# Kernel tuning notes

Measured on AMD Instinct MI355X. Metric: run time of the kernel, lower is better.

## Reference

```python
import jax, jax.numpy as jnp
import numpy as np

N, E, C, A, R = 8192, 65536, 64, 16, 8
DIMS = (1, 3, 5, 7)        # dims of l = 0..3 irrep blocks
IRDIM = sum(DIMS)          # 16
L = len(DIMS)              # 4 TP paths (0e x l -> l, 'uvu')
WN = L * C                 # conv_tp weight_numel = 256
HID = 64                   # radial MLP hidden width
AVG_NUM_NEIGH = 16.0


def setup_inputs() -> dict:
    key = jax.random.key(0)
    ks = jax.random.split(key, 18)
    f = lambda k, s: jax.random.normal(k, s, dtype=jnp.float32)
    return dict(
        node_attrs=f(ks[0], (N, A)),
        node_feats=f(ks[1], (N, C)),
        edge_attrs=f(ks[2], (E, IRDIM)),
        edge_feats=f(ks[3], (E, R)),
        edge_index=jax.random.randint(ks[4], (2, E), 0, N),
        magmom_node_inv_feats=f(ks[5], (N, R)),
        magmom_node_attrs=f(ks[6], (N, IRDIM)),
        # learned parameters (e3nn-style, no biases, 1/sqrt(fan_in) path norm)
        W_up=f(ks[7], (C, C)),
        W_r0=f(ks[8], (R + R, HID)),
        W_r1=f(ks[9], (HID, HID)),
        W_r2=f(ks[10], (HID, HID)),
        W_r3=f(ks[11], (HID, WN)),
        W_trans=f(ks[12], (WN, WN)),
        W_dens=f(ks[13], (R, 1)),
        W_lin=f(ks[14], (L, C, C)),
        W_mlin=f(ks[15], (L, C, C)),
        W_skip=f(ks[16], (L, C, A, C)),
        W_mskip=f(ks[17], (L, C, A, C)),
    )


def _per_l_linear(x, W):
    # equivariant Linear: independent channel-mixing per l block. x: [N,C,16]
    outs, o = [], 0
    for l, d in enumerate(DIMS):
        outs.append(jnp.einsum('ncm,cd->ndm', x[:, :, o:o + d], W[l]) / np.sqrt(C))
        o += d
    return jnp.concatenate(outs, axis=-1)


def _skip_tp(x, attrs, W):
    # FullyConnectedTensorProduct with scalar (0e) node attrs: (l x 0e -> l, 'uvw')
    outs, o = [], 0
    for l, d in enumerate(DIMS):
        outs.append(jnp.einsum('num,nv,uvw->nwm', x[:, :, o:o + d], attrs, W[l]) / np.sqrt(C * A))
        o += d
    return jnp.concatenate(outs, axis=-1)


def _weighted_tp(xj, attrs_e, w):
    # weighted TP of 0e node feats with lmax=3 attrs: per-edge 'uvu' weights.
    # xj: [E,C], attrs_e: [E,16], w: [E,L,C] -> [E,C,16]
    wf = jnp.repeat(w, np.array(DIMS), axis=1, total_repeat_length=IRDIM)  # [E,16,C]
    return xj[:, :, None] * attrs_e[:, None, :] * jnp.swapaxes(wf, 1, 2)


def reference(node_attrs, node_feats, edge_attrs, edge_feats, edge_index,
              magmom_node_inv_feats, magmom_node_attrs,
              W_up, W_r0, W_r1, W_r2, W_r3, W_trans, W_dens,
              W_lin, W_mlin, W_skip, W_mskip):
    sender, receiver = edge_index[0], edge_index[1]
    x = node_feats @ W_up / np.sqrt(C)                     # linear_up (0e)
    xj = x[sender]                                         # gather by sender
    h = jnp.concatenate([edge_feats, magmom_node_inv_feats[sender]], axis=-1)
    for W in (W_r0, W_r1, W_r2):                           # radial MLP (silu)
        h = jax.nn.silu(h @ W / np.sqrt(W.shape[0]))
    tp_w = (h @ W_r3 / np.sqrt(HID)).reshape(E, L, C)      # per-edge TP weights
    edge_density = jnp.tanh((edge_feats @ W_dens / np.sqrt(R)) ** 2)  # [E,1]
    mji = _weighted_tp(xj, edge_attrs, tp_w)               # [E,C,16]
    tp_w_m = (tp_w.reshape(E, WN) @ W_trans / np.sqrt(WN)).reshape(E, L, C)
    magmom_mji = _weighted_tp(xj, magmom_node_attrs[sender], tp_w_m)
    density = jax.ops.segment_sum(edge_density, receiver, num_segments=N)       # [N,1]
    message = jax.ops.segment_sum(mji, receiver, num_segments=N)                # [N,C,16]
    magmom_message = jax.ops.segment_sum(magmom_mji, receiver, num_segments=N)
    message = _per_l_linear(message, W_lin) / (density[:, :, None] + 1.0)
    message = _skip_tp(message, node_attrs, W_skip)
    magmom_message = _per_l_linear(magmom_message, W_mlin) / AVG_NUM_NEIGH
    magmom_message = _skip_tp(magmom_message, node_attrs, W_mskip)
    return message, magmom_message                         # each [N,C,16] (reshape_irreps layout)
```

## Files before the change

kernel.cpp:

```cpp
#include <hip/hip_runtime.h>

#define N_NODES 8192
#define N_EDGES 65536

typedef __attribute__((ext_vector_type(8))) short bf16x8;
typedef __attribute__((ext_vector_type(4))) float f32x4;

static __device__ __forceinline__ float bfl(unsigned v){ unsigned u=v<<16; float f; __builtin_memcpy(&f,&u,4); return f; }
static __device__ __forceinline__ float bfh(unsigned v){ unsigned u=v&0xffff0000u; float f; __builtin_memcpy(&f,&u,4); return f; }
static __device__ __forceinline__ float bfs(unsigned short h){ unsigned u=((unsigned)h)<<16; float f; __builtin_memcpy(&f,&u,4); return f; }
static __device__ __forceinline__ unsigned short f2bf(float f){ unsigned u; __builtin_memcpy(&u,&f,4); u += 0x7fffu + ((u>>16)&1u); return (unsigned short)(u>>16); }
static __device__ __forceinline__ unsigned pk(float a, float b){ return (unsigned)f2bf(a) | ((unsigned)f2bf(b)<<16); }
static __device__ __forceinline__ float silu_f(float v){ return v/(1.f+__expf(-v)); }

__global__ __launch_bounds__(256) void k_linup(const float* __restrict__ nf,
                                               const float* __restrict__ wup,
                                               float* __restrict__ x){
    __shared__ float s[4][64];
    const int t=threadIdx.x, wv=t>>6, lane=t&63;
    const int n=blockIdx.x*4+wv;
    s[wv][lane]=nf[(size_t)n*64+lane];
    __syncthreads();
    float acc=0.f;
    for(int c=0;c<64;++c) acc += s[wv][c]*wup[c*64+lane];
    x[(size_t)n*64+lane]=acc*0.125f;
}

__global__ __launch_bounds__(256) void k_wmlp(const float* __restrict__ wr0,
                                              const float* __restrict__ wr1,
                                              const float* __restrict__ wr2,
                                              unsigned short* __restrict__ w0f,
                                              unsigned short* __restrict__ w1f,
                                              unsigned short* __restrict__ w2f){
    const int b=blockIdx.x, t=threadIdx.x;
    #pragma unroll
    for(int z=0;z<2;++z){
        int idx=t*2+z;
        int lane=idx>>3, i=idx&7;
        if(b<4){
            int nt=b, k=(lane>>4)*8+i, n=nt*16+(lane&15);
            float v=(k<16)? wr0[k*64+n]*0.25f : 0.f;
            w0f[(nt*64+lane)*8+i]=f2bf(v);
        } else if(b<12){
            int q=b-4, nt=q>>1, ks=q&1;
            int k=ks*32+(lane>>4)*8+i, n=nt*16+(lane&15);
            w1f[((nt*2+ks)*64+lane)*8+i]=f2bf(wr1[k*64+n]*0.125f);
        } else {
            int q=b-12, nt=q>>1, ks=q&1;
            int k=ks*32+(lane>>4)*8+i, n=nt*16+(lane&15);
            w2f[((nt*2+ks)*64+lane)*8+i]=f2bf(wr2[k*64+n]*0.125f);
        }
    }
}

__global__ __launch_bounds__(256) void k_wtf(const float* __restrict__ wr3,
                                             const float* __restrict__ wtr,
                                             unsigned short* __restrict__ wtf){
    const int b=blockIdx.x;
    const int mt=b>>1, ks=b&1, t=threadIdx.x;
    #pragma unroll
    for(int z=0;z<2;++z){
        int idx=t*2+z;
        int lane=idx>>3, i=idx&7;
        int k=ks*32+(lane>>4)*8+i;
        int n=mt*16+(lane&15);
        int j=n>>3, s=n&7;
        float v;
        if(s<4) v=wr3[k*256+s*64+j]*0.125f;
        else {
            float acc=0.f;
            for(int kk=0;kk<256;++kk) acc+=wr3[k*256+kk]*wtr[kk*256+(s-4)*64+j];
            v=acc*(1.f/128.f);
        }
        wtf[((size_t)b*64+lane)*8+i]=f2bf(v);
    }
}

__global__ __launch_bounds__(256) void k_wwf(const float* __restrict__ wlin,
                                             const float* __restrict__ wmlin,
                                             const float* __restrict__ wskip,
                                             const float* __restrict__ wmskip,
                                             unsigned* __restrict__ wwf){
    const int b=blockIdx.x, ten=b>>8, lc=b&255, l=lc>>6, c=lc&63;
    const float* WL = ten? wmlin:wlin;
    const float* WS = ten? wmskip:wskip;
    const float scale = ten? (1.f/4096.f):(1.f/256.f);
    const int t=threadIdx.x, wg=t>>6, s=t&63, lane=s>>1, half=s&1;
    const int kg=lane>>4, w=wg*16+(lane&15);
    const int v0=kg*8+half*4;
    float a0=0,a1=0,a2=0,a3=0;
    for(int u=0;u<64;++u){
        float wl=WL[(l*64+c)*64+u];
        const float* wsp=&WS[(((l*64+u)*16+v0)*64)+w];
        a0+=wl*wsp[0]; a1+=wl*wsp[64]; a2+=wl*wsp[128]; a3+=wl*wsp[192];
    }
    size_t fi=(((size_t)ten*4+l)*64+c)*4+wg;
    unsigned* op=wwf + (fi*32+lane)*4 + half*2;
    op[0]=pk(a0*scale,a1*scale); op[1]=pk(a2*scale,a3*scale);
}

__global__ __launch_bounds__(256) void k_count(const int* __restrict__ recv, int* __restrict__ cnt){
    int e=blockIdx.x*256+threadIdx.x;
    atomicAdd(&cnt[recv[e]],1);
}
__global__ __launch_bounds__(1024) void k_scan(const int* __restrict__ cnt, int* __restrict__ rowptr, int* __restrict__ cur){
    __shared__ int s[1024];
    const int t=threadIdx.x;
    int c[8]; int sum=0;
    #pragma unroll
    for(int i=0;i<8;++i){ c[i]=cnt[t*8+i]; sum+=c[i]; }
    s[t]=sum; __syncthreads();
    for(int off=1;off<1024;off<<=1){
        int v=s[t]; int add=(t>=off)? s[t-off]:0;
        __syncthreads();
        s[t]=v+add;
        __syncthreads();
    }
    int run=s[t]-sum;
    #pragma unroll
    for(int i=0;i<8;++i){ rowptr[t*8+i]=run; cur[t*8+i]=run; run+=c[i]; }
    if(t==1023) rowptr[8192]=run;
}
__global__ __launch_bounds__(256) void k_scatter(const int* __restrict__ recv, int* __restrict__ cur, int* __restrict__ elist){
    int e=blockIdx.x*256+threadIdx.x;
    int r=recv[e];
    int p=atomicAdd(&cur[r],1);
    elist[p]=e;
}

__global__ __launch_bounds__(256) void k_edge2(
    const float* __restrict__ ef, const float* __restrict__ mminv,
    const float* __restrict__ mattr, const int* __restrict__ sender,
    const float* __restrict__ wdens,
    const uint4* __restrict__ w0f, const uint4* __restrict__ w1f,
    const uint4* __restrict__ w2f, const uint4* __restrict__ wtf,
    const float* __restrict__ x,
    unsigned short* __restrict__ wxc, float* __restrict__ man, float* __restrict__ ed)
{
    __shared__ unsigned short hA[4096];
    __shared__ unsigned short hB[4096];
    __shared__ float xs[64*68];
    const int t=threadIdx.x, lane=t&63, wv=t>>6;
    const int tile=blockIdx.x*64;

    {
        const int e=t>>2, q=t&3, ge=tile+e;
        const int s=sender[ge];
        const float4* xp=(const float4*)(x+(size_t)s*64+q*16);
        float4* xw=(float4*)&xs[e*68+q*16];
        xw[0]=xp[0]; xw[1]=xp[1]; xw[2]=xp[2]; xw[3]=xp[3];
        *(float4*)(man+(size_t)ge*16+q*4) = *(const float4*)(mattr+(size_t)s*16+q*4);
        const int se3=(e&7)<<3;
        if(q==0){
            float4 f0=*(const float4*)(ef+(size_t)ge*8);
            float4 f1=*(const float4*)(ef+(size_t)ge*8+4);
            uint4 o; o.x=pk(f0.x,f0.y); o.y=pk(f0.z,f0.w); o.z=pk(f1.x,f1.y); o.w=pk(f1.z,f1.w);
            *(uint4*)&hA[e*64 + (0^se3)]=o;
            float acc=f0.x*wdens[0]+f0.y*wdens[1]+f0.z*wdens[2]+f0.w*wdens[3]
                     +f1.x*wdens[4]+f1.y*wdens[5]+f1.z*wdens[6]+f1.w*wdens[7];
            acc*=0.35355339059327373f;
            float q2=acc*acc;
            float ex=__expf(2.f*q2);
            ed[ge]=1.f-2.f/(ex+1.f);
        } else if(q==1){
            float4 f0=*(const float4*)(mminv+(size_t)s*8);
            float4 f1=*(const float4*)(mminv+(size_t)s*8+4);
            uint4 o; o.x=pk(f0.x,f0.y); o.y=pk(f0.z,f0.w); o.z=pk(f1.x,f1.y); o.w=pk(f1.z,f1.w);
            *(uint4*)&hA[e*64 + (8^se3)]=o;
        } else if(q==2){
            *(uint4*)&hA[e*64 + (16^se3)]=make_uint4(0,0,0,0);
        } else {
            *(uint4*)&hA[e*64 + (24^se3)]=make_uint4(0,0,0,0);
        }
    }
    __syncthreads();

    const int arow=wv*16+(lane&15);
    const int akg=lane>>4;
    const int aswz=(arow&7)<<3;
    const int dcol=lane&15;
    const int drow0=wv*16+(lane>>4)*4;

    {
        uint4 av=*(const uint4*)&hA[arow*64+((akg*8)^aswz)];
        bf16x8 a; __builtin_memcpy(&a,&av,16);
        f32x4 d[4];
        #pragma unroll
        for(int nt=0;nt<4;++nt){
            uint4 bw=w0f[nt*64+lane];
            bf16x8 b; __builtin_memcpy(&b,&bw,16);
            f32x4 z={0.f,0.f,0.f,0.f};
            d[nt]=__builtin_amdgcn_mfma_f32_16x16x32_bf16(a,b,z,0,0,0);
        }
        #pragma unroll
        for(int nt=0;nt<4;++nt){
            #pragma unroll
            for(int r=0;r<4;++r){
                int e2=drow0+r, n=nt*16+dcol;
                hB[e2*64 + (n^((e2&7)<<3))]=f2bf(silu_f(d[nt][r]));
            }
        }
    }
    __syncthreads();

    {
        uint4 av0=*(const uint4*)&hB[arow*64+(((0+akg)*8)^aswz)];
        uint4 av1=*(const uint4*)&hB[arow*64+(((4+akg)*8)^aswz)];
        bf16x8 a0,a1; __builtin_memcpy(&a0,&av0,16); __builtin_memcpy(&a1,&av1,16);
        f32x4 d[4];
        #pragma unroll
        for(int nt=0;nt<4;++nt){
            uint4 bw0=w1f[(nt*2+0)*64+lane];
            uint4 bw1=w1f[(nt*2+1)*64+lane];
            bf16x8 b0,b1; __builtin_memcpy(&b0,&bw0,16); __builtin_memcpy(&b1,&bw1,16);
            f32x4 z={0.f,0.f,0.f,0.f};
            d[nt]=__builtin_amdgcn_mfma_f32_16x16x32_bf16(a0,b0,z,0,0,0);
            d[nt]=__builtin_amdgcn_mfma_f32_16x16x32_bf16(a1,b1,d[nt],0,0,0);
        }
        #pragma unroll
        for(int nt=0;nt<4;++nt){
            #pragma unroll
            for(int r=0;r<4;++r){
                int e2=drow0+r, n=nt*16+dcol;
                hA[e2*64 + (n^((e2&7)<<3))]=f2bf(silu_f(d[nt][r]));
            }
        }
    }
    __syncthreads();

    {
        uint4 av0=*(const uint4*)&hA[arow*64+(((0+akg)*8)^aswz)];
        uint4 av1=*(const uint4*)&hA[arow*64+(((4+akg)*8)^aswz)];
        bf16x8 a0,a1; __builtin_memcpy(&a0,&av0,16); __builtin_memcpy(&a1,&av1,16);
        f32x4 d[4];
        #pragma unroll
        for(int nt=0;nt<4;++nt){
            uint4 bw0=w2f[(nt*2+0)*64+lane];
            uint4 bw1=w2f[(nt*2+1)*64+lane];
            bf16x8 b0,b1; __builtin_memcpy(&b0,&bw0,16); __builtin_memcpy(&b1,&bw1,16);
            f32x4 z={0.f,0.f,0.f,0.f};
            d[nt]=__builtin_amdgcn_mfma_f32_16x16x32_bf16(a0,b0,z,0,0,0);
            d[nt]=__builtin_amdgcn_mfma_f32_16x16x32_bf16(a1,b1,d[nt],0,0,0);
        }
        #pragma unroll
        for(int nt=0;nt<4;++nt){
            #pragma unroll
            for(int r=0;r<4;++r){
                int e2=drow0+r, n=nt*16+dcol;
                hB[e2*64 + (n^((e2&7)<<3))]=f2bf(silu_f(d[nt][r]));
            }
        }
    }
    __syncthreads();

    {
        bf16x8 hb[4][2];
        #pragma unroll
        for(int nt2=0;nt2<4;++nt2){
            int erow=nt2*16+(lane&15);
            int esz=(erow&7)<<3;
            #pragma unroll
            for(int ks=0;ks<2;++ks){
                uint4 v=*(const uint4*)&hB[erow*64+(((ks*4+akg)*8)^esz)];
                __builtin_memcpy(&hb[nt2][ks],&v,16);
            }
        }
        const int g=lane>>4;
        const int jo=g>>1, sh=g&1;
        for(int mt=0;mt<8;++mt){
            int mtg=wv*8+mt;
            uint4 aw0=wtf[(mtg*2+0)*64+lane];
            uint4 aw1=wtf[(mtg*2+1)*64+lane];
            bf16x8 a0,a1; __builtin_memcpy(&a0,&aw0,16); __builtin_memcpy(&a1,&aw1,16);
            int j=mtg*2+jo;
            #pragma unroll
            for(int nt2=0;nt2<4;++nt2){
                f32x4 z={0.f,0.f,0.f,0.f};
                f32x4 d=__builtin_amdgcn_mfma_f32_16x16x32_bf16(a0,hb[nt2][0],z,0,0,0);
                d=__builtin_amdgcn_mfma_f32_16x16x32_bf16(a1,hb[nt2][1],d,0,0,0);
                int eloc=nt2*16+(lane&15);
                float xj=xs[eloc*68+j];
                uint2 o; o.x=pk(d[0]*xj,d[1]*xj); o.y=pk(d[2]*xj,d[3]*xj);
                *(uint2*)&wxc[((size_t)(tile+eloc)*64+j)*8+sh*4]=o;
            }
        }
    }
}

__global__ __launch_bounds__(256) void k_gather(
    const int* __restrict__ rowptr, const int* __restrict__ elist,
    const unsigned short* __restrict__ wxc, const float* __restrict__ ea,
    const float* __restrict__ man, const float* __restrict__ ed,
    float* __restrict__ out)
{
    const int t=threadIdx.x, wv=t>>6, lane=t&63;
    const int n=blockIdx.x*4+wv;
    const int r0=rowptr[n], r1=rowptr[n+1];
    float msg[16]; float mm[16];
    #pragma unroll
    for(int m=0;m<16;++m){ msg[m]=0.f; mm[m]=0.f; }
    float dens=0.f;
    for(int k=r0;k<r1;++k){
        int e=elist[k];
        uint4 r=*(const uint4*)(wxc+((size_t)e*64+lane)*8);
        float wx0=bfl(r.x),wx1=bfh(r.x),wx2=bfl(r.y),wx3=bfh(r.y);
        float wm0=bfl(r.z),wm1=bfh(r.z),wm2=bfl(r.w),wm3=bfh(r.w);
        dens+=ed[e];
        const float4* eap=(const float4*)(ea+(size_t)e*16);
        const float4* map=(const float4*)(man+(size_t)e*16);
        float4 A0=eap[0],A1=eap[1],A2=eap[2],A3=eap[3];
        float4 B0=map[0],B1=map[1],B2=map[2],B3=map[3];
        msg[0]+=wx0*A0.x;
        msg[1]+=wx1*A0.y;  msg[2]+=wx1*A0.z;  msg[3]+=wx1*A0.w;
        msg[4]+=wx2*A1.x;  msg[5]+=wx2*A1.y;  msg[6]+=wx2*A1.z;  msg[7]+=wx2*A1.w;  msg[8]+=wx2*A2.x;
        msg[9]+=wx3*A2.y;  msg[10]+=wx3*A2.z; msg[11]+=wx3*A2.w;
        msg[12]+=wx3*A3.x; msg[13]+=wx3*A3.y; msg[14]+=wx3*A3.z; msg[15]+=wx3*A3.w;
        mm[0]+=wm0*B0.x;
        mm[1]+=wm1*B0.y;  mm[2]+=wm1*B0.z;  mm[3]+=wm1*B0.w;
        mm[4]+=wm2*B1.x;  mm[5]+=wm2*B1.y;  mm[6]+=wm2*B1.z;  mm[7]+=wm2*B1.w;  mm[8]+=wm2*B2.x;
        mm[9]+=wm3*B2.y;  mm[10]+=wm3*B2.z; mm[11]+=wm3*B2.w;
        mm[12]+=wm3*B3.x; mm[13]+=wm3*B3.y; mm[14]+=wm3*B3.z; mm[15]+=wm3*B3.w;
    }
    float inv=1.f/(1.f+dens);
    float* mp=out+(size_t)n*1024+lane*16;
    ((float4*)mp)[0]=make_float4(msg[0]*inv,msg[1]*inv,msg[2]*inv,msg[3]*inv);
    ((float4*)mp)[1]=make_float4(msg[4]*inv,msg[5]*inv,msg[6]*inv,msg[7]*inv);
    ((float4*)mp)[2]=make_float4(msg[8]*inv,msg[9]*inv,msg[10]*inv,msg[11]*inv);
    ((float4*)mp)[3]=make_float4(msg[12]*inv,msg[13]*inv,msg[14]*inv,msg[15]*inv);
    float* qp=out+8388608+(size_t)n*1024+lane*16;
    ((float4*)qp)[0]=make_float4(mm[0],mm[1],mm[2],mm[3]);
    ((float4*)qp)[1]=make_float4(mm[4],mm[5],mm[6],mm[7]);
    ((float4*)qp)[2]=make_float4(mm[8],mm[9],mm[10],mm[11]);
    ((float4*)qp)[3]=make_float4(mm[12],mm[13],mm[14],mm[15]);
}

__global__ __launch_bounds__(256) void k_final6(const float* __restrict__ attrs,
                                                const unsigned* __restrict__ wwf,
                                                float* __restrict__ out){
    __shared__ unsigned short msgS[64*16*8];
    const int blk=blockIdx.x;
    const int half=blk&1;
    const int rest=blk>>1;
    const int ten=rest>>9, nb=(rest&511)*16;
    float* base=out+(size_t)ten*8388608;
    const int t=threadIdx.x, lane=t&63, wg=t>>6;
    const int L0=half;

    const float4* src=(const float4*)(base+(size_t)nb*1024);
    #pragma unroll
    for(int i=0;i<8;++i){
        int tau=i*256+t;
        int n=tau>>7, rem=tau&127, c=rem>>1, qq=rem&1;
        float4 f=src[(n<<8)+(c<<2)+half*2+qq];
        unsigned* dst=(unsigned*)&msgS[(c*16+n)*8+qq*4];
        dst[0]=pk(f.x,f.y); dst[1]=pk(f.z,f.w);
    }
    bf16x8 afrag;
    {
        int nloc=lane&15, kg=lane>>4;
        if(kg<2){
            const float* ap=attrs+(size_t)(nb+nloc)*16+kg*8;
            #pragma unroll
            for(int i=0;i<8;++i) afrag[i]=(short)f2bf(ap[i]);
        } else {
            #pragma unroll
            for(int i=0;i<8;++i) afrag[i]=0;
        }
    }
    __syncthreads();

    const int g4=(lane>>4)*4;
    const int colw=lane&15;
    float acc[4][8];
    #pragma unroll
    for(int r=0;r<4;++r)
        #pragma unroll
        for(int m=0;m<8;++m) acc[r][m]=0.f;

    const uint4* wwf4=(const uint4*)wwf;
    uint4 bcur[3], bnxt[3];
    #pragma unroll
    for(int li=0;li<3;++li){
        int fi=(((ten*4+L0+li)*64+0)*4+wg);
        bcur[li]=wwf4[fi*32+(lane&31)];
    }

    constexpr int LI0[8]={0,1,1,1,2,2,2,2};
    constexpr int LI1[8]={1,2,2,2,2,2,2,2};

    for(int c=0;c<64;++c){
        if(c<63){
            #pragma unroll
            for(int li=0;li<3;++li){
                int fi=(((ten*4+L0+li)*64+(c+1))*4+wg);
                bnxt[li]=wwf4[fi*32+(lane&31)];
            }
        }
        f32x4 d[3];
        #pragma unroll
        for(int li=0;li<3;++li){
            bf16x8 b; __builtin_memcpy(&b,&bcur[li],16);
            f32x4 z={0.f,0.f,0.f,0.f};
            d[li]=__builtin_amdgcn_mfma_f32_16x16x32_bf16(afrag,b,z,0,0,0);
        }
        #pragma unroll
        for(int r=0;r<4;++r){
            uint4 h=*(const uint4*)&msgS[(c*16+g4+r)*8];
            unsigned wd[4]={h.x,h.y,h.z,h.w};
            #pragma unroll
            for(int m=0;m<8;++m){
                float mv = (m&1)? bfh(wd[m>>1]) : bfl(wd[m>>1]);
                float dv = half? d[LI1[m]][r] : d[LI0[m]][r];
                acc[r][m] += mv * dv;
            }
        }
        if(c<63){
            #pragma unroll
            for(int li=0;li<3;++li) bcur[li]=bnxt[li];
        }
    }
    const int w=wg*16+colw;
    #pragma unroll
    for(int r=0;r<4;++r){
        float* op=base+(size_t)(nb+g4+r)*1024+w*16+half*8;
        ((float4*)op)[0]=make_float4(acc[r][0],acc[r][1],acc[r][2],acc[r][3]);
        ((float4*)op)[1]=make_float4(acc[r][4],acc[r][5],acc[r][6],acc[r][7]);
    }
}

extern "C" void kernel_launch(void* const* d_in, const int* in_sizes, int n_in,
                              void* d_out, int out_size, void* d_ws, size_t ws_size,
                              hipStream_t stream) {
    const float* node_attrs=(const float*)d_in[0];
    const float* node_feats=(const float*)d_in[1];
    const float* edge_attrs=(const float*)d_in[2];
    const float* edge_feats=(const float*)d_in[3];
    const int*   eidx_in  =(const int*)  d_in[4];
    const int*   sender   =eidx_in;
    const int*   recv     =eidx_in+N_EDGES;
    const float* mminv    =(const float*)d_in[5];
    const float* mattr    =(const float*)d_in[6];
    const float* wup      =(const float*)d_in[7];
    const float* wr0      =(const float*)d_in[8];
    const float* wr1      =(const float*)d_in[9];
    const float* wr2      =(const float*)d_in[10];
    const float* wr3      =(const float*)d_in[11];
    const float* wtr      =(const float*)d_in[12];
    const float* wdens    =(const float*)d_in[13];
    const float* wlin     =(const float*)d_in[14];
    const float* wmlin    =(const float*)d_in[15];
    const float* wskip    =(const float*)d_in[16];
    const float* wmskip   =(const float*)d_in[17];

    char* ws=(char*)d_ws;
    float*          x     =(float*)(ws+0);
    unsigned short* wxc   =(unsigned short*)(ws+2097152);
    float*          man   =(float*)(ws+69206016);
    float*          ed    =(float*)(ws+73400320);
    unsigned short* wtf   =(unsigned short*)(ws+73662464);
    unsigned*       wwf   =(unsigned*)(ws+73728000);
    unsigned short* w0f   =(unsigned short*)(ws+75825152);
    unsigned short* w1f   =(unsigned short*)(ws+75829248);
    unsigned short* w2f   =(unsigned short*)(ws+75837440);
    int*            cnt   =(int*)(ws+75845632);
    int*            rowptr=(int*)(ws+75878400);
    int*            cur   =(int*)(ws+75911296);
    int*            elist =(int*)(ws+75944064);
    if(ws_size < (size_t)76206208) return;

    float* out=(float*)d_out;

    hipMemsetAsync(cnt,0,32768,stream);
    k_linup  <<<dim3(2048),dim3(256),0,stream>>>(node_feats,wup,x);
    k_wmlp   <<<dim3(20),  dim3(256),0,stream>>>(wr0,wr1,wr2,w0f,w1f,w2f);
    k_wtf    <<<dim3(64),  dim3(256),0,stream>>>(wr3,wtr,wtf);
    k_wwf    <<<dim3(512), dim3(256),0,stream>>>(wlin,wmlin,wskip,wmskip,wwf);
    k_count  <<<dim3(256), dim3(256),0,stream>>>(recv,cnt);
    k_scan   <<<dim3(1),   dim3(1024),0,stream>>>(cnt,rowptr,cur);
    k_scatter<<<dim3(256), dim3(256),0,stream>>>(recv,cur,elist);
    k_edge2  <<<dim3(1024),dim3(256),0,stream>>>(edge_feats,mminv,mattr,sender,wdens,
                                                 (const uint4*)w0f,(const uint4*)w1f,
                                                 (const uint4*)w2f,(const uint4*)wtf,
                                                 x,wxc,man,ed);
    k_gather <<<dim3(2048),dim3(256),0,stream>>>(rowptr,elist,wxc,edge_attrs,man,ed,out);
    k_final6 <<<dim3(2048),dim3(256),0,stream>>>(node_attrs,wwf,out);
}
```

Measured before the change: 259.2 us.

## Drop per-edge magmom attr copy, precompute W_r3·W_trans, restructure final skip kernel

Measured after the change: 242.1 us. 1.07x faster.

```diff
diff --git a/kernel.cpp b/kernel.cpp
--- a/kernel.cpp
+++ b/kernel.cpp
@@ -53,8 +53,17 @@
     }
 }
 
+__global__ __launch_bounds__(256) void k_w3t(const float* __restrict__ wr3,
+                                             const float* __restrict__ wtr,
+                                             float* __restrict__ wt){
+    const int k=blockIdx.x, n=threadIdx.x;
+    float acc=0.f;
+    for(int kk=0;kk<256;++kk) acc += wr3[k*256+kk]*wtr[kk*256+n];
+    wt[k*256+n]=acc;
+}
+
 __global__ __launch_bounds__(256) void k_wtf(const float* __restrict__ wr3,
-                                             const float* __restrict__ wtr,
+                                             const float* __restrict__ wt,
                                              unsigned short* __restrict__ wtf){
     const int b=blockIdx.x;
     const int mt=b>>1, ks=b&1, t=threadIdx.x;
@@ -65,13 +74,8 @@
         int k=ks*32+(lane>>4)*8+i;
         int n=mt*16+(lane&15);
         int j=n>>3, s=n&7;
-        float v;
-        if(s<4) v=wr3[k*256+s*64+j]*0.125f;
-        else {
-            float acc=0.f;
-            for(int kk=0;kk<256;++kk) acc+=wr3[k*256+kk]*wtr[kk*256+(s-4)*64+j];
-            v=acc*(1.f/128.f);
-        }
+        float v = (s<4)? wr3[k*256+s*64+j]*0.125f
+                       : wt[k*256+(s-4)*64+j]*(1.f/128.f);
         wtf[((size_t)b*64+lane)*8+i]=f2bf(v);
     }
 }
@@ -130,12 +134,12 @@
 
 __global__ __launch_bounds__(256) void k_edge2(
     const float* __restrict__ ef, const float* __restrict__ mminv,
-    const float* __restrict__ mattr, const int* __restrict__ sender,
+    const int* __restrict__ sender,
     const float* __restrict__ wdens,
     const uint4* __restrict__ w0f, const uint4* __restrict__ w1f,
     const uint4* __restrict__ w2f, const uint4* __restrict__ wtf,
     const float* __restrict__ x,
-    unsigned short* __restrict__ wxc, float* __restrict__ man, float* __restrict__ ed)
+    unsigned short* __restrict__ wxc, float* __restrict__ ed)
 {
     __shared__ unsigned short hA[4096];
     __shared__ unsigned short hB[4096];
@@ -149,7 +153,6 @@
         const float4* xp=(const float4*)(x+(size_t)s*64+q*16);
         float4* xw=(float4*)&xs[e*68+q*16];
         xw[0]=xp[0]; xw[1]=xp[1]; xw[2]=xp[2]; xw[3]=xp[3];
-        *(float4*)(man+(size_t)ge*16+q*4) = *(const float4*)(mattr+(size_t)s*16+q*4);
         const int se3=(e&7)<<3;
         if(q==0){
             float4 f0=*(const float4*)(ef+(size_t)ge*8);
@@ -290,7 +293,8 @@
 __global__ __launch_bounds__(256) void k_gather(
     const int* __restrict__ rowptr, const int* __restrict__ elist,
     const unsigned short* __restrict__ wxc, const float* __restrict__ ea,
-    const float* __restrict__ man, const float* __restrict__ ed,
+    const float* __restrict__ mattr, const int* __restrict__ sender,
+    const float* __restrict__ ed,
     float* __restrict__ out)
 {
     const int t=threadIdx.x, wv=t>>6, lane=t&63;
@@ -303,11 +307,12 @@
     for(int k=r0;k<r1;++k){
         int e=elist[k];
         uint4 r=*(const uint4*)(wxc+((size_t)e*64+lane)*8);
+        int s=sender[e];
         float wx0=bfl(r.x),wx1=bfh(r.x),wx2=bfl(r.y),wx3=bfh(r.y);
         float wm0=bfl(r.z),wm1=bfh(r.z),wm2=bfl(r.w),wm3=bfh(r.w);
         dens+=ed[e];
         const float4* eap=(const float4*)(ea+(size_t)e*16);
-        const float4* map=(const float4*)(man+(size_t)e*16);
+        const float4* map=(const float4*)(mattr+(size_t)s*16);
         float4 A0=eap[0],A1=eap[1],A2=eap[2],A3=eap[3];
         float4 B0=map[0],B1=map[1],B2=map[2],B3=map[3];
         msg[0]+=wx0*A0.x;
@@ -334,7 +339,40 @@
     ((float4*)qp)[3]=make_float4(mm[12],mm[13],mm[14],mm[15]);
 }
 
-__global__ __launch_bounds__(256) void k_final6(const float* __restrict__ attrs,
+#define STEP0_(v0,v1,v2, cc) { \
+    _Pragma("unroll") \
+    for(int r_=0;r_<4;++r_){ \
+        uint4 h_=*(const uint4*)&msgS[(((cc)*16+g4+r_))*8]; \
+        float dr0_=v0[r_], dr1_=v1[r_], dr2_=v2[r_]; \
+        acc[r_][0]+=bfl(h_.x)*dr0_; \
+        acc[r_][1]+=bfh(h_.x)*dr1_; \
+        acc[r_][2]+=bfl(h_.y)*dr1_; \
+        acc[r_][3]+=bfh(h_.y)*dr1_; \
+        acc[r_][4]+=bfl(h_.z)*dr2_; \
+        acc[r_][5]+=bfh(h_.z)*dr2_; \
+        acc[r_][6]+=bfl(h_.w)*dr2_; \
+        acc[r_][7]+=bfh(h_.w)*dr2_; \
+    } }
+#define STEP1_(v0,v1, cc) { \
+    _Pragma("unroll") \
+    for(int r_=0;r_<4;++r_){ \
+        uint4 h_=*(const uint4*)&msgS[(((cc)*16+g4+r_))*8]; \
+        float dr0_=v0[r_], dr1_=v1[r_]; \
+        acc[r_][0]+=bfl(h_.x)*dr0_; \
+        acc[r_][1]+=bfh(h_.x)*dr1_; \
+        acc[r_][2]+=bfl(h_.y)*dr1_; \
+        acc[r_][3]+=bfh(h_.y)*dr1_; \
+        acc[r_][4]+=bfl(h_.z)*dr1_; \
+        acc[r_][5]+=bfh(h_.z)*dr1_; \
+        acc[r_][6]+=bfl(h_.w)*dr1_; \
+        acc[r_][7]+=bfh(h_.w)*dr1_; \
+    } }
+#define MFMA1_(o, b) { \
+    bf16x8 f_; __builtin_memcpy(&f_,&(b),16); \
+    f32x4 z_={0.f,0.f,0.f,0.f}; \
+    o=__builtin_amdgcn_mfma_f32_16x16x32_bf16(afrag,f_,z_,0,0,0); }
+
+__global__ __launch_bounds__(256) void k_final8(const float* __restrict__ attrs,
                                                 const unsigned* __restrict__ wwf,
                                                 float* __restrict__ out){
     __shared__ unsigned short msgS[64*16*8];
@@ -344,7 +382,6 @@
     const int ten=rest>>9, nb=(rest&511)*16;
     float* base=out+(size_t)ten*8388608;
     const int t=threadIdx.x, lane=t&63, wg=t>>6;
-    const int L0=half;
 
     const float4* src=(const float4*)(base+(size_t)nb*1024);
     #pragma unroll
@@ -370,7 +407,6 @@
     __syncthreads();
 
     const int g4=(lane>>4)*4;
-    const int colw=lane&15;
     float acc[4][8];
     #pragma unroll
     for(int r=0;r<4;++r)
@@ -378,48 +414,46 @@
         for(int m=0;m<8;++m) acc[r][m]=0.f;
 
     const uint4* wwf4=(const uint4*)wwf;
-    uint4 bcur[3], bnxt[3];
-    #pragma unroll
-    for(int li=0;li<3;++li){
-        int fi=(((ten*4+L0+li)*64+0)*4+wg);
-        bcur[li]=wwf4[fi*32+(lane&31)];
-    }
-
-    constexpr int LI0[8]={0,1,1,1,2,2,2,2};
-    constexpr int LI1[8]={1,2,2,2,2,2,2,2};
-
-    for(int c=0;c<64;++c){
-        if(c<63){
-            #pragma unroll
-            for(int li=0;li<3;++li){
-                int fi=(((ten*4+L0+li)*64+(c+1))*4+wg);
-                bnxt[li]=wwf4[fi*32+(lane&31)];
-            }
-        }
-        f32x4 d[3];
-        #pragma unroll
-        for(int li=0;li<3;++li){
-            bf16x8 b; __builtin_memcpy(&b,&bcur[li],16);
-            f32x4 z={0.f,0.f,0.f,0.f};
-            d[li]=__builtin_amdgcn_mfma_f32_16x16x32_bf16(afrag,b,z,0,0,0);
-        }
-        #pragma unroll
-        for(int r=0;r<4;++r){
-            uint4 h=*(const uint4*)&msgS[(c*16+g4+r)*8];
-            unsigned wd[4]={h.x,h.y,h.z,h.w};
-            #pragma unroll
-            for(int m=0;m<8;++m){
-                float mv = (m&1)? bfh(wd[m>>1]) : bfl(wd[m>>1]);
-                float dv = half? d[LI1[m]][r] : d[LI0[m]][r];
-                acc[r][m] += mv * dv;
-            }
-        }
-        if(c<63){
-            #pragma unroll
-            for(int li=0;li<3;++li) bcur[li]=bnxt[li];
-        }
-    }
-    const int w=wg*16+colw;
+    const int l31=lane&31;
+
+    if(half==0){
+        const uint4* p0=wwf4+((size_t)((ten*4+0)*64)*4+wg)*32+l31;
+        const uint4* p1=wwf4+((size_t)((ten*4+1)*64)*4+wg)*32+l31;
+        const uint4* p2=wwf4+((size_t)((ten*4+2)*64)*4+wg)*32+l31;
+        uint4 A0=p0[0], A1=p1[0], A2=p2[0];
+        uint4 B0=p0[128], B1=p1[128], B2=p2[128];
+        f32x4 dA0,dA1,dA2, dB0,dB1,dB2;
+        MFMA1_(dA0,A0); MFMA1_(dA1,A1); MFMA1_(dA2,A2);
+        for(int c=0;c<64;c+=2){
+            const int cA=(c+2<64)? c+2 : 63;
+            const int cB=(c+3<64)? c+3 : 63;
+            A0=p0[cA*128]; A1=p1[cA*128]; A2=p2[cA*128];
+            MFMA1_(dB0,B0); MFMA1_(dB1,B1); MFMA1_(dB2,B2);
+            STEP0_(dA0,dA1,dA2, c);
+            B0=p0[cB*128]; B1=p1[cB*128]; B2=p2[cB*128];
+            MFMA1_(dA0,A0); MFMA1_(dA1,A1); MFMA1_(dA2,A2);
+            STEP0_(dB0,dB1,dB2, c+1);
+        }
+    } else {
+        const uint4* p0=wwf4+((size_t)((ten*4+2)*64)*4+wg)*32+l31;
+        const uint4* p1=wwf4+((size_t)((ten*4+3)*64)*4+wg)*32+l31;
+        uint4 A0=p0[0], A1=p1[0];
+        uint4 B0=p0[128], B1=p1[128];
+        f32x4 dA0,dA1, dB0,dB1;
+        MFMA1_(dA0,A0); MFMA1_(dA1,A1);
+        for(int c=0;c<64;c+=2){
+            const int cA=(c+2<64)? c+2 : 63;
+            const int cB=(c+3<64)? c+3 : 63;
+            A0=p0[cA*128]; A1=p1[cA*128];
+            MFMA1_(dB0,B0); MFMA1_(dB1,B1);
+            STEP1_(dA0,dA1, c);
+            B0=p0[cB*128]; B1=p1[cB*128];
+            MFMA1_(dA0,A0); MFMA1_(dA1,A1);
+            STEP1_(dB0,dB1, c+1);
+        }
+    }
+
+    const int w=wg*16+(lane&15);
     #pragma unroll
     for(int r=0;r<4;++r){
         float* op=base+(size_t)(nb+g4+r)*1024+w*16+half*8;
@@ -455,7 +489,7 @@
     char* ws=(char*)d_ws;
     float*          x     =(float*)(ws+0);
     unsigned short* wxc   =(unsigned short*)(ws+2097152);
-    float*          man   =(float*)(ws+69206016);
+    float*          wt    =(float*)(ws+69206016);
     float*          ed    =(float*)(ws+73400320);
     unsigned short* wtf   =(unsigned short*)(ws+73662464);
     unsigned*       wwf   =(unsigned*)(ws+73728000);
@@ -473,15 +507,16 @@
     hipMemsetAsync(cnt,0,32768,stream);
     k_linup  <<<dim3(2048),dim3(256),0,stream>>>(node_feats,wup,x);
     k_wmlp   <<<dim3(20),  dim3(256),0,stream>>>(wr0,wr1,wr2,w0f,w1f,w2f);
-    k_wtf    <<<dim3(64),  dim3(256),0,stream>>>(wr3,wtr,wtf);
+    k_w3t    <<<dim3(64),  dim3(256),0,stream>>>(wr3,wtr,wt);
+    k_wtf    <<<dim3(64),  dim3(256),0,stream>>>(wr3,wt,wtf);
     k_wwf    <<<dim3(512), dim3(256),0,stream>>>(wlin,wmlin,wskip,wmskip,wwf);
     k_count  <<<dim3(256), dim3(256),0,stream>>>(recv,cnt);
     k_scan   <<<dim3(1),   dim3(1024),0,stream>>>(cnt,rowptr,cur);
     k_scatter<<<dim3(256), dim3(256),0,stream>>>(recv,cur,elist);
-    k_edge2  <<<dim3(1024),dim3(256),0,stream>>>(edge_feats,mminv,mattr,sender,wdens,
+    k_edge2  <<<dim3(1024),dim3(256),0,stream>>>(edge_feats,mminv,sender,wdens,
                                                  (const uint4*)w0f,(const uint4*)w1f,
                                                  (const uint4*)w2f,(const uint4*)wtf,
-                                                 x,wxc,man,ed);
-    k_gather <<<dim3(2048),dim3(256),0,stream>>>(rowptr,elist,wxc,edge_attrs,man,ed,out);
-    k_final6 <<<dim3(2048),dim3(256),0,stream>>>(node_attrs,wwf,out);
-}
+                                                 x,wxc,ed);
+    k_gather <<<dim3(2048),dim3(256),0,stream>>>(rowptr,elist,wxc,edge_attrs,mattr,sender,ed,out);
+    k_final8 <<<dim3(2048),dim3(256),0,stream>>>(node_attrs,wwf,out);
+}
```
